# Performance work log

Hardware: AMD Instinct MI355X
Metric: run time of the kernel (lower is better)

Reference implementation:

```python
import jax, jax.numpy as jnp
import numpy as np

MARGIN = 1.0
BATCH = 512
NFEAT = 128
NTRIP = 1024


def setup_inputs() -> dict:
    key = jax.random.key(0)
    k1, k2 = jax.random.split(key)
    embeddings = jax.random.normal(k1, (BATCH, NFEAT), dtype=jnp.float32)
    triplets = jax.random.randint(k2, (NTRIP, 3), 0, BATCH, dtype=jnp.int64)
    return {"embeddings": embeddings, "triplets": triplets}


def _triplet_loss(embeddings, triplets, margin):
    pivot = embeddings[triplets[:, 0]]
    positives = embeddings[triplets[:, 1]]
    negatives = embeddings[triplets[:, 2]]
    ap = jnp.sum((pivot - positives) ** 2, axis=1)
    an = jnp.sum((pivot - negatives) ** 2, axis=1)
    return jnp.mean(jax.nn.relu(ap - an + margin))


def _dist_corr_loss(embeddings):
    # embeddings: [B, n]; treat each feature column as a 1-D sample.
    B, n = embeddings.shape
    X = embeddings.T  # [n, B]
    # Per-column pairwise L1 distance matrices: [n, B, B]
    D = jnp.abs(X[:, :, None] - X[:, None, :])
    m = jnp.mean(D, axis=1)                      # [n, B] row/col means (D symmetric)
    g = jnp.mean(m, axis=1)                      # [n] grand means
    A = D - m[:, None, :] - m[:, :, None] + g[:, None, None]  # double-centered
    # S[i, j] = mean(A_i * A_j) over the B*B entries
    S = jnp.einsum('iab,jab->ij', A, A) / (B * B)
    diag = jnp.diagonal(S)                       # mean(A_i^2) = varA_i^2 pre-sqrt
    # dCov(i,j) = sqrt(S_ij); dCorr = dCov / sqrt(sqrt(S_ii)*sqrt(S_jj))
    denom = jnp.sqrt(jnp.sqrt(diag)[:, None] * jnp.sqrt(diag)[None, :])
    corr = jnp.sqrt(S) / denom                   # [n, n]
    iu, ju = jnp.triu_indices(n, k=1)
    return jnp.mean(corr[iu, ju])


def reference(embeddings, triplets):
    triplet_loss = _triplet_loss(embeddings, triplets, MARGIN)
    corr_loss = _dist_corr_loss(embeddings)
    return triplet_loss + corr_loss
```

## Files before the change

kernel.cpp:

```cpp
#include <hip/hip_runtime.h>
#include <hip/hip_bf16.h>

#define B_    512
#define F_    128
#define NTRIP 1024
#define MARGIN 1.0f
#define NBLK  32
#define NPAIRB 132
#define NFOLD  4
#define PREP  130

#define OFF_M    0
#define OFF_MT   65536
#define OFF_G    131072
#define OFF_TL   131200
#define OFF_SQ   131216
#define OFF_PART 147600

typedef __attribute__((ext_vector_type(8))) short bf16x8;
typedef __attribute__((ext_vector_type(4))) float f32x4;

#define LDS_ROW 20

__device__ inline unsigned int bf16r(float f) {
    unsigned int u = __float_as_uint(f);
    u += 0x7FFFu + ((u >> 16) & 1u);
    return u >> 16;
}

__global__ __launch_bounds__(512)
void k1_prep_pair(const float* __restrict__ emb, const int* __restrict__ trip,
                  float* __restrict__ m, float* __restrict__ mT,
                  float* __restrict__ g, float* __restrict__ tl,
                  float* __restrict__ sq, float* __restrict__ out,
                  unsigned short* __restrict__ part) {
    __shared__ __align__(16) unsigned int dt[4 * F_ * LDS_ROW];
    const int bid = blockIdx.x;
    const int t   = threadIdx.x;

    if (bid < PREP) {
        if (bid < F_) {
            float*  x    = (float*)dt;
            float4* red4 = (float4*)((float*)dt + 512);
            const int i = bid;
            if (i == 0 && t == 0) out[0] = 0.f;
            x[t] = emb[t * F_ + i];
            __syncthreads();
            const float xa = x[t];
            float s0 = 0.f, s1 = 0.f, s2 = 0.f, s3 = 0.f;
            for (int b = 0; b < B_; b += 4) {
                s0 += fabsf(xa - x[b]);
                s1 += fabsf(xa - x[b + 1]);
                s2 += fabsf(xa - x[b + 2]);
                s3 += fabsf(xa - x[b + 3]);
            }
            float s = (s0 + s1) + (s2 + s3);
            float mv = s * (1.f / B_);
            m[i * B_ + t]  = mv;
            mT[t * F_ + i] = mv;
            red4[t] = make_float4(s, xa, xa * xa, mv * mv);
            __syncthreads();
            for (int sh = 256; sh > 0; sh >>= 1) {
                if (t < sh) {
                    float4 a = red4[t], b = red4[t + sh];
                    red4[t] = make_float4(a.x + b.x, a.y + b.y, a.z + b.z, a.w + b.w);
                }
                __syncthreads();
            }
            if (t == 0) {
                float4 r = red4[0];
                const float Bf = (float)B_;
                float gi = r.x * (1.f / (Bf * Bf));
                g[i] = gi;
                float DD  = 2.f * Bf * r.z - 2.f * r.y * r.y;
                float Sii = DD * (1.f / (Bf * Bf)) - (2.f / Bf) * r.w + gi * gi;
                sq[i] = sqrtf(sqrtf(fmaxf(Sii, 0.f)));
            }
        } else {
            float* red = (float*)dt;
            const int tt = (bid - F_) * 512 + t;
            int a = trip[3 * tt]     & (B_ - 1);
            int p = trip[3 * tt + 1] & (B_ - 1);
            int n = trip[3 * tt + 2] & (B_ - 1);
            const float4* ea = (const float4*)(emb + a * F_);
            const float4* ep = (const float4*)(emb + p * F_);
            const float4* en = (const float4*)(emb + n * F_);
            float ap = 0.f, an = 0.f;
            #pragma unroll 8
            for (int f4 = 0; f4 < F_ / 4; ++f4) {
                float4 va = ea[f4], vp = ep[f4], vn = en[f4];
                float d;
                d = va.x - vp.x; ap = fmaf(d, d, ap);
                d = va.y - vp.y; ap = fmaf(d, d, ap);
                d = va.z - vp.z; ap = fmaf(d, d, ap);
                d = va.w - vp.w; ap = fmaf(d, d, ap);
                d = va.x - vn.x; an = fmaf(d, d, an);
                d = va.y - vn.y; an = fmaf(d, d, an);
                d = va.z - vn.z; an = fmaf(d, d, an);
                d = va.w - vn.w; an = fmaf(d, d, an);
            }
            float l = fmaxf(ap - an + MARGIN, 0.f);
            red[t] = l;
            __syncthreads();
            for (int sh = 256; sh > 0; sh >>= 1) {
                if (t < sh) red[t] += red[t + sh];
                __syncthreads();
            }
            if (t == 0) tl[bid - F_] = red[0];
        }
        return;
    }

    const int pbp = bid - PREP;
    const int lane = t & 63;
    const int w    = t >> 6;
    const int wr   = w >> 1;
    const int wc   = w & 1;
    const int i    = t & 127;
    const int pg   = t >> 7;
    const int fr_row = lane & 15;
    const int fr_k4  = (lane >> 4) * 4;

    f32x4 acc[2][4];
    #pragma unroll
    for (int q = 0; q < 2; ++q)
        #pragma unroll
        for (int c = 0; c < 4; ++c) acc[q][c] = (f32x4)(0.f);

    for (int u = 0; u < NFOLD; ++u) {
        const int L = pbp + u * NPAIRB;
        int ba = 0, rem = L;
        while (rem >= NBLK - ba) { rem -= NBLK - ba; ++ba; }
        const int bb = ba + rem;
        const bool diag = (ba == bb);

        float xb[16];
        #pragma unroll
        for (int b = 0; b < 16; ++b) xb[b] = emb[(bb * 16 + b) * F_ + i];

        #pragma unroll
        for (int h = 0; h < 2; ++h) {
            const float xa0 = emb[(ba * 16 + h * 8 + pg * 2 + 0) * F_ + i];
            const float xa1 = emb[(ba * 16 + h * 8 + pg * 2 + 1) * F_ + i];
            if (h | u) __syncthreads();
            #pragma unroll
            for (int ar2 = 0; ar2 < 2; ++ar2) {
                const float xa = ar2 ? xa1 : xa0;
                const int pa = h * 8 + pg * 2 + ar2;
                unsigned int pk[8];
                #pragma unroll
                for (int q = 0; q < 8; ++q) {
                    float d0 = fabsf(xa - xb[2 * q]);
                    float d1 = fabsf(xa - xb[2 * q + 1]);
                    if (diag && pa >= 2 * q)     d0 = 0.f;
                    if (diag && pa >= 2 * q + 1) d1 = 0.f;
                    pk[q] = bf16r(d0) | (bf16r(d1) << 16);
                }
                unsigned int* dst = &dt[pg * (F_ * LDS_ROW) + i * LDS_ROW + ar2 * 8];
                *reinterpret_cast<uint4*>(dst)     = make_uint4(pk[0], pk[1], pk[2], pk[3]);
                *reinterpret_cast<uint4*>(dst + 4) = make_uint4(pk[4], pk[5], pk[6], pk[7]);
            }
            __syncthreads();
            #pragma unroll
            for (int c = 0; c < 4; ++c) {
                const unsigned int* base = &dt[c * (F_ * LDS_ROW)];
                const bf16x8 fA0 = *reinterpret_cast<const bf16x8*>(
                    &base[((wr * 2 + 0) * 16 + fr_row) * LDS_ROW + fr_k4]);
                const bf16x8 fA1 = *reinterpret_cast<const bf16x8*>(
                    &base[((wr * 2 + 1) * 16 + fr_row) * LDS_ROW + fr_k4]);
                #pragma unroll
                for (int cg = 0; cg < 4; ++cg) {
                    const bf16x8 fB = *reinterpret_cast<const bf16x8*>(
                        &base[((wc * 4 + cg) * 16 + fr_row) * LDS_ROW + fr_k4]);
                    acc[0][cg] = __builtin_amdgcn_mfma_f32_16x16x32_bf16(fA0, fB, acc[0][cg], 0, 0, 0);
                    acc[1][cg] = __builtin_amdgcn_mfma_f32_16x16x32_bf16(fA1, fB, acc[1][cg], 0, 0, 0);
                }
            }
        }
    }

    unsigned short* dstp = part + (size_t)pbp * (F_ * F_);
    const int cj = lane & 15;
    const int rsub = (lane >> 4) * 4;
    #pragma unroll
    for (int q = 0; q < 2; ++q)
        #pragma unroll
        for (int cg = 0; cg < 4; ++cg)
            #pragma unroll
            for (int r = 0; r < 4; ++r)
                dstp[((wr * 2 + q) * 16 + rsub + r) * F_ + (wc * 4 + cg) * 16 + cj] =
                    (unsigned short)bf16r(acc[q][cg][r]);
}

__global__ __launch_bounds__(512)
void k2_srow_final(const unsigned short* __restrict__ part,
                   const float* __restrict__ m, const float* __restrict__ mT,
                   const float* __restrict__ g, const float* __restrict__ sq,
                   const float* __restrict__ tl, float* __restrict__ out) {
    __shared__ float shT[16][64];
    __shared__ float shM[8][64];
    __shared__ float smi[B_];
    __shared__ float red[64];
    const int bid = blockIdx.x;
    const int i   = bid >> 1;
    const int jh  = bid & 1;
    const int t   = threadIdx.x;

    const int dw = t & 31;
    const int sl = t >> 5;
    const int cnt = (sl < 4) ? 9 : 8;
    const int st  = sl * 8 + (sl < 4 ? sl : 4);
    const unsigned int* src = reinterpret_cast<const unsigned int*>(part)
                            + i * 64 + jh * 32 + dw;
    float tlo = 0.f, thi = 0.f;
    for (int s = st; s < st + cnt; ++s) {
        unsigned int v = src[(size_t)s * 8192];
        tlo += __uint_as_float(v << 16);
        thi += __uint_as_float(v & 0xFFFF0000u);
    }
    shT[sl][dw * 2]     = tlo;
    shT[sl][dw * 2 + 1] = thi;
    smi[t] = m[i * B_ + t];
    __syncthreads();

    const int jl = t & 63;
    const int j  = jh * 64 + jl;
    const int q8 = t >> 6;
    float md = 0.f;
    const float* mta = mT + (size_t)(q8 * 64) * F_ + j;
    const float* mia = smi + q8 * 64;
    #pragma unroll 8
    for (int a = 0; a < 64; ++a) md = fmaf(mia[a], mta[(size_t)a * F_], md);
    shM[q8][jl] = md;
    __syncthreads();

    if (t < 64) {
        float T = 0.f;
        #pragma unroll
        for (int s = 0; s < 16; ++s) T += shT[s][t];
        float mdj = 0.f;
        #pragma unroll
        for (int s = 0; s < 8; ++s) mdj += shM[s][t];
        const int jj = jh * 64 + t;
        float Sij = 2.f * T * (1.f / ((float)B_ * (float)B_))
                  - (2.f / (float)B_) * mdj
                  + g[i] * g[jj];
        float c = 0.f;
        if (jj > i) c = sqrtf(fmaxf(Sij, 0.f)) / (sq[i] * sq[jj]);
        red[t] = c;
    }
    __syncthreads();
    for (int sh = 32; sh > 0; sh >>= 1) {
        if (t < sh) red[t] += red[t + sh];
        __syncthreads();
    }
    if (t == 0) {
        float v = red[0] * (1.f / 8128.f);
        if (bid == 0) v += (tl[0] + tl[1]) * (1.f / (float)NTRIP);
        atomicAdd(out, v);
    }
}

extern "C" void kernel_launch(void* const* d_in, const int* in_sizes, int n_in,
                              void* d_out, int out_size, void* d_ws, size_t ws_size,
                              hipStream_t stream) {
    const float* emb = (const float*)d_in[0];
    const int*   trp = (const int*)d_in[1];
    float* ws  = (float*)d_ws;
    float* m   = ws + OFF_M;
    float* mT  = ws + OFF_MT;
    float* g   = ws + OFF_G;
    float* tl  = ws + OFF_TL;
    float* sq  = ws + OFF_SQ;
    unsigned short* part = (unsigned short*)(ws + OFF_PART);
    float* out = (float*)d_out;

    k1_prep_pair  <<<PREP + NPAIRB, 512, 0, stream>>>(emb, trp, m, mT, g, tl, sq, out, part);
    k2_srow_final <<<256, 512, 0, stream>>>(part, m, mT, g, sq, tl, out);
}
```

Before: 38.61 us.

## Prefetch next fold's embeddings, reorder blocks so pair work starts first, unroll k2 loads

Measured after the change: 39.33 us. About the same (+1.9%).

```diff
diff --git a/kernel.cpp b/kernel.cpp
--- a/kernel.cpp
+++ b/kernel.cpp
@@ -38,27 +38,28 @@
     const int bid = blockIdx.x;
     const int t   = threadIdx.x;
 
-    if (bid < PREP) {
-        if (bid < F_) {
+    if (bid >= NPAIRB) {
+        const int pbb = bid - NPAIRB;
+        if (pbb < F_) {
             float*  x    = (float*)dt;
             float4* red4 = (float4*)((float*)dt + 512);
-            const int i = bid;
+            const int i = pbb;
             if (i == 0 && t == 0) out[0] = 0.f;
             x[t] = emb[t * F_ + i];
             __syncthreads();
-            const float xa = x[t];
+            const float xav = x[t];
             float s0 = 0.f, s1 = 0.f, s2 = 0.f, s3 = 0.f;
             for (int b = 0; b < B_; b += 4) {
-                s0 += fabsf(xa - x[b]);
-                s1 += fabsf(xa - x[b + 1]);
-                s2 += fabsf(xa - x[b + 2]);
-                s3 += fabsf(xa - x[b + 3]);
+                s0 += fabsf(xav - x[b]);
+                s1 += fabsf(xav - x[b + 1]);
+                s2 += fabsf(xav - x[b + 2]);
+                s3 += fabsf(xav - x[b + 3]);
             }
             float s = (s0 + s1) + (s2 + s3);
             float mv = s * (1.f / B_);
             m[i * B_ + t]  = mv;
             mT[t * F_ + i] = mv;
-            red4[t] = make_float4(s, xa, xa * xa, mv * mv);
+            red4[t] = make_float4(s, xav, xav * xav, mv * mv);
             __syncthreads();
             for (int sh = 256; sh > 0; sh >>= 1) {
                 if (t < sh) {
@@ -78,7 +79,7 @@
             }
         } else {
             float* red = (float*)dt;
-            const int tt = (bid - F_) * 512 + t;
+            const int tt = (pbb - F_) * 512 + t;
             int a = trip[3 * tt]     & (B_ - 1);
             int p = trip[3 * tt + 1] & (B_ - 1);
             int n = trip[3 * tt + 2] & (B_ - 1);
@@ -106,12 +107,12 @@
                 if (t < sh) red[t] += red[t + sh];
                 __syncthreads();
             }
-            if (t == 0) tl[bid - F_] = red[0];
+            if (t == 0) tl[pbb - F_] = red[0];
         }
         return;
     }
 
-    const int pbp = bid - PREP;
+    const int pbp = bid;
     const int lane = t & 63;
     const int w    = t >> 6;
     const int wr   = w >> 1;
@@ -121,37 +122,44 @@
     const int fr_row = lane & 15;
     const int fr_k4  = (lane >> 4) * 4;
 
-    f32x4 acc[2][4];
-    #pragma unroll
-    for (int q = 0; q < 2; ++q)
-        #pragma unroll
-        for (int c = 0; c < 4; ++c) acc[q][c] = (f32x4)(0.f);
-
+    int baA[NFOLD], bbA[NFOLD];
+    #pragma unroll
     for (int u = 0; u < NFOLD; ++u) {
-        const int L = pbp + u * NPAIRB;
+        int L = pbp + u * NPAIRB;
         int ba = 0, rem = L;
         while (rem >= NBLK - ba) { rem -= NBLK - ba; ++ba; }
-        const int bb = ba + rem;
-        const bool diag = (ba == bb);
-
-        float xb[16];
-        #pragma unroll
-        for (int b = 0; b < 16; ++b) xb[b] = emb[(bb * 16 + b) * F_ + i];
-
+        baA[u] = ba; bbA[u] = ba + rem;
+    }
+
+    f32x4 acc[2][4];
+    #pragma unroll
+    for (int q = 0; q < 2; ++q)
+        #pragma unroll
+        for (int c = 0; c < 4; ++c) acc[q][c] = (f32x4)(0.f);
+
+    float xb[2][16], xa[2][4];
+    #pragma unroll
+    for (int b = 0; b < 16; ++b) xb[0][b] = emb[(bbA[0] * 16 + b) * F_ + i];
+    #pragma unroll
+    for (int k = 0; k < 4; ++k)
+        xa[0][k] = emb[(baA[0] * 16 + (k >> 1) * 8 + pg * 2 + (k & 1)) * F_ + i];
+
+    #pragma unroll
+    for (int u = 0; u < NFOLD; ++u) {
+        const int cu = u & 1, nx = cu ^ 1;
+        const bool diag = (baA[u] == bbA[u]);
         #pragma unroll
         for (int h = 0; h < 2; ++h) {
-            const float xa0 = emb[(ba * 16 + h * 8 + pg * 2 + 0) * F_ + i];
-            const float xa1 = emb[(ba * 16 + h * 8 + pg * 2 + 1) * F_ + i];
             if (h | u) __syncthreads();
             #pragma unroll
             for (int ar2 = 0; ar2 < 2; ++ar2) {
-                const float xa = ar2 ? xa1 : xa0;
+                const float xav = xa[cu][h * 2 + ar2];
                 const int pa = h * 8 + pg * 2 + ar2;
                 unsigned int pk[8];
                 #pragma unroll
                 for (int q = 0; q < 8; ++q) {
-                    float d0 = fabsf(xa - xb[2 * q]);
-                    float d1 = fabsf(xa - xb[2 * q + 1]);
+                    float d0 = fabsf(xav - xb[cu][2 * q]);
+                    float d1 = fabsf(xav - xb[cu][2 * q + 1]);
                     if (diag && pa >= 2 * q)     d0 = 0.f;
                     if (diag && pa >= 2 * q + 1) d1 = 0.f;
                     pk[q] = bf16r(d0) | (bf16r(d1) << 16);
@@ -159,6 +167,14 @@
                 unsigned int* dst = &dt[pg * (F_ * LDS_ROW) + i * LDS_ROW + ar2 * 8];
                 *reinterpret_cast<uint4*>(dst)     = make_uint4(pk[0], pk[1], pk[2], pk[3]);
                 *reinterpret_cast<uint4*>(dst + 4) = make_uint4(pk[4], pk[5], pk[6], pk[7]);
+            }
+            if (h == 1 && u < NFOLD - 1) {
+                #pragma unroll
+                for (int b = 0; b < 16; ++b)
+                    xb[nx][b] = emb[(bbA[u + 1] * 16 + b) * F_ + i];
+                #pragma unroll
+                for (int k = 0; k < 4; ++k)
+                    xa[nx][k] = emb[(baA[u + 1] * 16 + (k >> 1) * 8 + pg * 2 + (k & 1)) * F_ + i];
             }
             __syncthreads();
             #pragma unroll
@@ -208,15 +224,17 @@
 
     const int dw = t & 31;
     const int sl = t >> 5;
-    const int cnt = (sl < 4) ? 9 : 8;
-    const int st  = sl * 8 + (sl < 4 ? sl : 4);
     const unsigned int* src = reinterpret_cast<const unsigned int*>(part)
                             + i * 64 + jh * 32 + dw;
     float tlo = 0.f, thi = 0.f;
-    for (int s = st; s < st + cnt; ++s) {
-        unsigned int v = src[(size_t)s * 8192];
-        tlo += __uint_as_float(v << 16);
-        thi += __uint_as_float(v & 0xFFFF0000u);
+    #pragma unroll
+    for (int k = 0; k < 9; ++k) {
+        const int s = sl + 16 * k;
+        if (s < NPAIRB) {
+            unsigned int v = src[(size_t)s * 8192];
+            tlo += __uint_as_float(v << 16);
+            thi += __uint_as_float(v & 0xFFFF0000u);
+        }
     }
     shT[sl][dw * 2]     = tlo;
     shT[sl][dw * 2 + 1] = thi;
@@ -275,6 +293,6 @@
     unsigned short* part = (unsigned short*)(ws + OFF_PART);
     float* out = (float*)d_out;
 
-    k1_prep_pair  <<<PREP + NPAIRB, 512, 0, stream>>>(emb, trp, m, mT, g, tl, sq, out, part);
+    k1_prep_pair  <<<NPAIRB + PREP, 512, 0, stream>>>(emb, trp, m, mT, g, tl, sq, out, part);
     k2_srow_final <<<256, 512, 0, stream>>>(part, m, mT, g, sq, tl, out);
 }
```
